# Optimization experiments

Measured on AMD Instinct MI355X. Metric: run time of the kernel, lower is better.

## Reference

```python
import jax, jax.numpy as jnp
import numpy as np

N = 100000
E = 1600000
F_IN = 64
F_OUT = 64
K = 3


def setup_inputs() -> dict:
    key = jax.random.key(0)
    k1, k2, k3, k4, k5 = jax.random.split(key, 5)
    x = jax.random.normal(k1, (N, F_IN), dtype=jnp.float32)
    rows = jnp.sort(jax.random.randint(k2, (E,), 0, N, dtype=jnp.int32))
    cols = jax.random.randint(k3, (E,), 0, N, dtype=jnp.int32)
    vals = jax.random.uniform(k4, (E,), dtype=jnp.float32)
    # xavier-uniform-ish weights
    limit = float(np.sqrt(6.0 / (F_IN + F_OUT)))
    weight = jax.random.uniform(k5, (K, F_IN, F_OUT), dtype=jnp.float32,
                                minval=-limit, maxval=limit)
    bias = jnp.zeros((F_OUT,), dtype=jnp.float32)
    return {"x": x, "rows": rows, "cols": cols, "vals": vals,
            "weight": weight, "bias": bias}


def _spmm(vals, rows, cols, h):
    # adj @ h with adj in COO form: out[i] = sum_{e: rows[e]==i} vals[e] * h[cols[e]]
    return jax.ops.segment_sum(vals[:, None] * h[cols], rows, num_segments=N)


def reference(x, rows, cols, vals, weight, bias):
    Tx_0 = x                              # T_0(L) x = x
    Tx_1 = _spmm(vals, rows, cols, x)     # T_1(L) x = L x
    out = Tx_0 @ weight[0] + Tx_1 @ weight[1]
    for k in range(2, K):                 # Chebyshev recurrence (K is small/static)
        Tx_2 = 2.0 * _spmm(vals, rows, cols, Tx_1) - Tx_0
        out = out + Tx_2 @ weight[k]
        Tx_0, Tx_1 = Tx_1, Tx_2
    return out + bias
```

## Files before the change

kernel.cpp:

```cpp
#include <hip/hip_runtime.h>

constexpr int NN = 100000;
constexpr int NE = 1600000;
constexpr int F  = 64;

typedef short bf16x8 __attribute__((ext_vector_type(8)));
typedef float f32x4  __attribute__((ext_vector_type(4)));

__device__ __forceinline__ float bf_lo(unsigned u) { return __uint_as_float(u << 16); }
__device__ __forceinline__ float bf_hi(unsigned u) { return __uint_as_float(u & 0xFFFF0000u); }
__device__ __forceinline__ unsigned pack_bf16(float a, float b) {
    unsigned ua = __float_as_uint(a);
    unsigned ub = __float_as_uint(b);
    ua = (ua + 0x7FFFu + ((ua >> 16) & 1u)) >> 16;
    ub = (ub + 0x7FFFu + ((ub >> 16) & 1u)) & 0xFFFF0000u;
    return ua | ub;
}

__global__ __launch_bounds__(256)
void build_row_ptr_k(const int* __restrict__ rows, int* __restrict__ row_ptr) {
    int r = blockIdx.x * 256 + threadIdx.x;
    if (r > NN) return;
    int lo = 0, hi = NE;
    while (lo < hi) {
        int mid = (lo + hi) >> 1;
        if (rows[mid] < r) lo = mid + 1; else hi = mid;
    }
    row_ptr[r] = lo;
}

__global__ __launch_bounds__(256)
void cvt_x_k(const float* __restrict__ x, ushort* __restrict__ xb) {
    int tid = blockIdx.x * 256 + threadIdx.x;
    if (tid >= NN * F / 8) return;
    const float4* p = (const float4*)x + (size_t)tid * 2;
    float4 a = p[0], b = p[1];
    uint4 o = make_uint4(pack_bf16(a.x, a.y), pack_bf16(a.z, a.w),
                         pack_bf16(b.x, b.y), pack_bf16(b.z, b.w));
    ((uint4*)xb)[tid] = o;
}

__global__ __launch_bounds__(256)
void cvt_w_k(const float* __restrict__ w, ushort* __restrict__ wt) {
    int tid = blockIdx.x * 256 + threadIdx.x;
    if (tid >= 192 * 64) return;
    int k = tid >> 6, n = tid & 63;
    unsigned u = __float_as_uint(w[tid]);
    u = (u + 0x7FFFu + ((u >> 16) & 1u)) >> 16;
    wt[n * 192 + k] = (ushort)u;
}

template<bool SECOND>
__global__ __launch_bounds__(256)
void spmm_k(const int* __restrict__ row_ptr, const int* __restrict__ cols,
            const float* __restrict__ vals, const ushort* __restrict__ src,
            const ushort* __restrict__ x0, ushort* __restrict__ dst) {
    const int lane = threadIdx.x & 63;
    const int i = blockIdx.x * 4 + (threadIdx.x >> 6);
    if (i >= NN) return;
    const int e0 = row_ptr[i];
    const int e1 = row_ptr[i + 1];
    const int fgrp = lane & 7;
    const int egrp = lane >> 3;
    float acc[8] = {};
    for (int base = e0; base < e1; base += 64) {
        const int n = min(64, e1 - base);
        int c = 0; float v = 0.f;
        if (lane < n) {
            c = cols[base + lane];
            v = vals[base + lane];
        }
        const int steps = (n + 7) >> 3;
        #pragma unroll 4
        for (int s = 0; s < steps; ++s) {
            int   cj = __shfl(c, s * 8 + egrp);
            float vj = __shfl(v, s * 8 + egrp);
            uint4 raw = *(const uint4*)(src + (size_t)cj * F + fgrp * 8);
            acc[0] += vj * bf_lo(raw.x); acc[1] += vj * bf_hi(raw.x);
            acc[2] += vj * bf_lo(raw.y); acc[3] += vj * bf_hi(raw.y);
            acc[4] += vj * bf_lo(raw.z); acc[5] += vj * bf_hi(raw.z);
            acc[6] += vj * bf_lo(raw.w); acc[7] += vj * bf_hi(raw.w);
        }
    }
    #pragma unroll
    for (int m = 8; m < 64; m <<= 1)
        #pragma unroll
        for (int t = 0; t < 8; ++t)
            acc[t] += __shfl_xor(acc[t], m);
    if (egrp == 0) {
        float r[8];
        if (SECOND) {
            uint4 xr = *(const uint4*)(x0 + (size_t)i * F + fgrp * 8);
            r[0] = 2.f * acc[0] - bf_lo(xr.x); r[1] = 2.f * acc[1] - bf_hi(xr.x);
            r[2] = 2.f * acc[2] - bf_lo(xr.y); r[3] = 2.f * acc[3] - bf_hi(xr.y);
            r[4] = 2.f * acc[4] - bf_lo(xr.z); r[5] = 2.f * acc[5] - bf_hi(xr.z);
            r[6] = 2.f * acc[6] - bf_lo(xr.w); r[7] = 2.f * acc[7] - bf_hi(xr.w);
        } else {
            #pragma unroll
            for (int t = 0; t < 8; ++t) r[t] = acc[t];
        }
        uint4 o = make_uint4(pack_bf16(r[0], r[1]), pack_bf16(r[2], r[3]),
                             pack_bf16(r[4], r[5]), pack_bf16(r[6], r[7]));
        *(uint4*)(dst + (size_t)i * F + fgrp * 8) = o;
    }
}

__global__ __launch_bounds__(256)
void dense_k(const ushort* __restrict__ xb, const ushort* __restrict__ t1,
             const ushort* __restrict__ t2, const ushort* __restrict__ wt,
             const float* __restrict__ bias, float* __restrict__ out) {
    const int tid  = threadIdx.x;
    const int lane = tid & 63;
    const int wv   = tid >> 6;
    const int row0 = blockIdx.x * 64 + wv * 16;
    const int m    = lane & 15;
    const int quad = lane >> 4;
    int arow = row0 + m;
    if (arow >= NN) arow = NN - 1;

    f32x4 acc[4] = {};
    #pragma unroll
    for (int kb = 0; kb < 6; ++kb) {
        const int kbase = kb * 32;
        const ushort* seg = (kb < 2) ? xb : (kb < 4) ? t1 : t2;
        const int off = (kbase & 63) + quad * 8;
        bf16x8 a = *(const bf16x8*)(seg + (size_t)arow * F + off);
        #pragma unroll
        for (int t = 0; t < 4; ++t) {
            const int n = t * 16 + m;
            bf16x8 b = *(const bf16x8*)(wt + (size_t)n * 192 + kbase + quad * 8);
            acc[t] = __builtin_amdgcn_mfma_f32_16x16x32_bf16(a, b, acc[t], 0, 0, 0);
        }
    }
    #pragma unroll
    for (int t = 0; t < 4; ++t) {
        const int col = t * 16 + m;
        const float bv = bias[col];
        #pragma unroll
        for (int r = 0; r < 4; ++r) {
            const int grow = row0 + quad * 4 + r;
            if (grow < NN) out[(size_t)grow * F + col] = acc[t][r] + bv;
        }
    }
}

extern "C" void kernel_launch(void* const* d_in, const int* in_sizes, int n_in,
                              void* d_out, int out_size, void* d_ws, size_t ws_size,
                              hipStream_t stream) {
    const float* x    = (const float*)d_in[0];
    const int*   rows = (const int*)  d_in[1];
    const int*   cols = (const int*)  d_in[2];
    const float* vals = (const float*)d_in[3];
    const float* w    = (const float*)d_in[4];
    const float* bias = (const float*)d_in[5];
    float* out = (float*)d_out;

    char* ws = (char*)d_ws;
    int* row_ptr = (int*)ws;
    size_t off = (((size_t)(NN + 1) * sizeof(int)) + 255) & ~(size_t)255;
    ushort* xb  = (ushort*)(ws + off);
    ushort* t1b = xb  + (size_t)NN * F;
    ushort* t2b = t1b + (size_t)NN * F;
    ushort* wt  = t2b + (size_t)NN * F;

    build_row_ptr_k<<<(NN + 1 + 255) / 256, 256, 0, stream>>>(rows, row_ptr);
    cvt_x_k<<<(NN * F / 8 + 255) / 256, 256, 0, stream>>>(x, xb);
    cvt_w_k<<<(192 * 64 + 255) / 256, 256, 0, stream>>>(w, wt);
    spmm_k<false><<<NN / 4, 256, 0, stream>>>(row_ptr, cols, vals, xb,  nullptr, t1b);
    spmm_k<true ><<<NN / 4, 256, 0, stream>>>(row_ptr, cols, vals, t1b, xb,      t2b);
    dense_k<<<(NN + 63) / 64, 256, 0, stream>>>(xb, t1b, t2b, wt, bias, out);
}
```

Baseline: 213.6 us.

## Fuse prep kernels, map eight rows per wave in SpMM, stage dense output via LDS

Merges the x conversion, row_ptr construction and weight transpose into one prep kernel, and builds row_ptr by scanning edges for row boundaries instead of one binary search per row. SpMM now gives each 8-lane group its own row and loops to the wave's maximum degree with masked edges. This removes the cross-lane reduction and raises parallelism for the average degree of 16, at the cost of load imbalance between rows of different degree. The dense kernel stages results through shared memory so each output row is written as contiguous float4 stores.

```diff
diff --git a/kernel.cpp b/kernel.cpp
--- a/kernel.cpp
+++ b/kernel.cpp
@@ -17,37 +17,36 @@
     return ua | ub;
 }
 
-__global__ __launch_bounds__(256)
-void build_row_ptr_k(const int* __restrict__ rows, int* __restrict__ row_ptr) {
-    int r = blockIdx.x * 256 + threadIdx.x;
-    if (r > NN) return;
-    int lo = 0, hi = NE;
-    while (lo < hi) {
-        int mid = (lo + hi) >> 1;
-        if (rows[mid] < r) lo = mid + 1; else hi = mid;
-    }
-    row_ptr[r] = lo;
-}
+constexpr int B_CVT = NN * F / 8 / 256;
+constexpr int B_RP  = NE / 256;
+constexpr int B_W   = 192 * 64 / 256;
 
 __global__ __launch_bounds__(256)
-void cvt_x_k(const float* __restrict__ x, ushort* __restrict__ xb) {
-    int tid = blockIdx.x * 256 + threadIdx.x;
-    if (tid >= NN * F / 8) return;
-    const float4* p = (const float4*)x + (size_t)tid * 2;
-    float4 a = p[0], b = p[1];
-    uint4 o = make_uint4(pack_bf16(a.x, a.y), pack_bf16(a.z, a.w),
-                         pack_bf16(b.x, b.y), pack_bf16(b.z, b.w));
-    ((uint4*)xb)[tid] = o;
-}
-
-__global__ __launch_bounds__(256)
-void cvt_w_k(const float* __restrict__ w, ushort* __restrict__ wt) {
-    int tid = blockIdx.x * 256 + threadIdx.x;
-    if (tid >= 192 * 64) return;
-    int k = tid >> 6, n = tid & 63;
-    unsigned u = __float_as_uint(w[tid]);
-    u = (u + 0x7FFFu + ((u >> 16) & 1u)) >> 16;
-    wt[n * 192 + k] = (ushort)u;
+void prep_k(const float* __restrict__ x, ushort* __restrict__ xb,
+            const int* __restrict__ rows, int* __restrict__ row_ptr,
+            const float* __restrict__ w, ushort* __restrict__ wt) {
+    const int b = blockIdx.x;
+    if (b < B_CVT) {
+        int tid = b * 256 + threadIdx.x;
+        const float4* p = (const float4*)x + (size_t)tid * 2;
+        float4 a = p[0], c = p[1];
+        uint4 o = make_uint4(pack_bf16(a.x, a.y), pack_bf16(a.z, a.w),
+                             pack_bf16(c.x, c.y), pack_bf16(c.z, c.w));
+        ((uint4*)xb)[tid] = o;
+    } else if (b < B_CVT + B_RP) {
+        int e = (b - B_CVT) * 256 + threadIdx.x;
+        int r1 = rows[e];
+        int r2 = (e == NE - 1) ? NN : rows[e + 1];
+        for (int r = r1 + 1; r <= r2; ++r) row_ptr[r] = e + 1;
+        if (e == 0)
+            for (int r = 0; r <= r1; ++r) row_ptr[r] = 0;
+    } else {
+        int tid = (b - B_CVT - B_RP) * 256 + threadIdx.x;
+        int k = tid >> 6, n = tid & 63;
+        unsigned u = __float_as_uint(w[tid]);
+        u = (u + 0x7FFFu + ((u >> 16) & 1u)) >> 16;
+        wt[n * 192 + k] = (ushort)u;
+    }
 }
 
 template<bool SECOND>
@@ -56,59 +55,54 @@
             const float* __restrict__ vals, const ushort* __restrict__ src,
             const ushort* __restrict__ x0, ushort* __restrict__ dst) {
     const int lane = threadIdx.x & 63;
-    const int i = blockIdx.x * 4 + (threadIdx.x >> 6);
-    if (i >= NN) return;
-    const int e0 = row_ptr[i];
-    const int e1 = row_ptr[i + 1];
     const int fgrp = lane & 7;
-    const int egrp = lane >> 3;
+    const int g    = lane >> 3;
+    const int r    = (blockIdx.x * 4 + (threadIdx.x >> 6)) * 8 + g;
+    const int e0 = row_ptr[r];
+    const int e1 = row_ptr[r + 1];
+    const int deg = e1 - e0;
+    int maxdeg = deg;
+    maxdeg = max(maxdeg, __shfl_xor(maxdeg, 8));
+    maxdeg = max(maxdeg, __shfl_xor(maxdeg, 16));
+    maxdeg = max(maxdeg, __shfl_xor(maxdeg, 32));
+
     float acc[8] = {};
-    for (int base = e0; base < e1; base += 64) {
-        const int n = min(64, e1 - base);
-        int c = 0; float v = 0.f;
-        if (lane < n) {
-            c = cols[base + lane];
-            v = vals[base + lane];
-        }
-        const int steps = (n + 7) >> 3;
-        #pragma unroll 4
-        for (int s = 0; s < steps; ++s) {
-            int   cj = __shfl(c, s * 8 + egrp);
-            float vj = __shfl(v, s * 8 + egrp);
-            uint4 raw = *(const uint4*)(src + (size_t)cj * F + fgrp * 8);
-            acc[0] += vj * bf_lo(raw.x); acc[1] += vj * bf_hi(raw.x);
-            acc[2] += vj * bf_lo(raw.y); acc[3] += vj * bf_hi(raw.y);
-            acc[4] += vj * bf_lo(raw.z); acc[5] += vj * bf_hi(raw.z);
-            acc[6] += vj * bf_lo(raw.w); acc[7] += vj * bf_hi(raw.w);
-        }
+    #pragma unroll 2
+    for (int s = 0; s < maxdeg; ++s) {
+        const bool act = s < deg;
+        int ec = act ? (e0 + s) : (e1 - 1);
+        ec = ec < 0 ? 0 : ec;
+        const int   cj = cols[ec];
+        const float vv = vals[ec];
+        const float vj = act ? vv : 0.f;
+        uint4 raw = *(const uint4*)(src + (size_t)cj * F + fgrp * 8);
+        acc[0] += vj * bf_lo(raw.x); acc[1] += vj * bf_hi(raw.x);
+        acc[2] += vj * bf_lo(raw.y); acc[3] += vj * bf_hi(raw.y);
+        acc[4] += vj * bf_lo(raw.z); acc[5] += vj * bf_hi(raw.z);
+        acc[6] += vj * bf_lo(raw.w); acc[7] += vj * bf_hi(raw.w);
     }
-    #pragma unroll
-    for (int m = 8; m < 64; m <<= 1)
+
+    float o[8];
+    if (SECOND) {
+        uint4 xr = *(const uint4*)(x0 + (size_t)r * F + fgrp * 8);
+        o[0] = 2.f * acc[0] - bf_lo(xr.x); o[1] = 2.f * acc[1] - bf_hi(xr.x);
+        o[2] = 2.f * acc[2] - bf_lo(xr.y); o[3] = 2.f * acc[3] - bf_hi(xr.y);
+        o[4] = 2.f * acc[4] - bf_lo(xr.z); o[5] = 2.f * acc[5] - bf_hi(xr.z);
+        o[6] = 2.f * acc[6] - bf_lo(xr.w); o[7] = 2.f * acc[7] - bf_hi(xr.w);
+    } else {
         #pragma unroll
-        for (int t = 0; t < 8; ++t)
-            acc[t] += __shfl_xor(acc[t], m);
-    if (egrp == 0) {
-        float r[8];
-        if (SECOND) {
-            uint4 xr = *(const uint4*)(x0 + (size_t)i * F + fgrp * 8);
-            r[0] = 2.f * acc[0] - bf_lo(xr.x); r[1] = 2.f * acc[1] - bf_hi(xr.x);
-            r[2] = 2.f * acc[2] - bf_lo(xr.y); r[3] = 2.f * acc[3] - bf_hi(xr.y);
-            r[4] = 2.f * acc[4] - bf_lo(xr.z); r[5] = 2.f * acc[5] - bf_hi(xr.z);
-            r[6] = 2.f * acc[6] - bf_lo(xr.w); r[7] = 2.f * acc[7] - bf_hi(xr.w);
-        } else {
-            #pragma unroll
-            for (int t = 0; t < 8; ++t) r[t] = acc[t];
-        }
-        uint4 o = make_uint4(pack_bf16(r[0], r[1]), pack_bf16(r[2], r[3]),
-                             pack_bf16(r[4], r[5]), pack_bf16(r[6], r[7]));
-        *(uint4*)(dst + (size_t)i * F + fgrp * 8) = o;
+        for (int t = 0; t < 8; ++t) o[t] = acc[t];
     }
+    uint4 ov = make_uint4(pack_bf16(o[0], o[1]), pack_bf16(o[2], o[3]),
+                          pack_bf16(o[4], o[5]), pack_bf16(o[6], o[7]));
+    *(uint4*)(dst + (size_t)r * F + fgrp * 8) = ov;
 }
 
 __global__ __launch_bounds__(256)
 void dense_k(const ushort* __restrict__ xb, const ushort* __restrict__ t1,
              const ushort* __restrict__ t2, const ushort* __restrict__ wt,
              const float* __restrict__ bias, float* __restrict__ out) {
+    __shared__ float lds[4][16 * 68];
     const int tid  = threadIdx.x;
     const int lane = tid & 63;
     const int wv   = tid >> 6;
@@ -132,15 +126,24 @@
             acc[t] = __builtin_amdgcn_mfma_f32_16x16x32_bf16(a, b, acc[t], 0, 0, 0);
         }
     }
+
+    float* sl = lds[wv];
     #pragma unroll
     for (int t = 0; t < 4; ++t) {
-        const int col = t * 16 + m;
-        const float bv = bias[col];
+        const float bv = bias[t * 16 + m];
         #pragma unroll
-        for (int r = 0; r < 4; ++r) {
-            const int grow = row0 + quad * 4 + r;
-            if (grow < NN) out[(size_t)grow * F + col] = acc[t][r] + bv;
-        }
+        for (int rr = 0; rr < 4; ++rr)
+            sl[(quad * 4 + rr) * 68 + t * 16 + m] = acc[t][rr] + bv;
+    }
+    __syncthreads();
+    const int m4 = (lane & 15) * 4;
+    #pragma unroll
+    for (int p = 0; p < 4; ++p) {
+        const int rl = p * 4 + (lane >> 4);
+        const int grow = row0 + rl;
+        f32x4 v = *(const f32x4*)(sl + rl * 68 + m4);
+        if (grow < NN)
+            *(f32x4*)(out + (size_t)grow * F + m4) = v;
     }
 }
 
@@ -163,10 +166,8 @@
     ushort* t2b = t1b + (size_t)NN * F;
     ushort* wt  = t2b + (size_t)NN * F;
 
-    build_row_ptr_k<<<(NN + 1 + 255) / 256, 256, 0, stream>>>(rows, row_ptr);
-    cvt_x_k<<<(NN * F / 8 + 255) / 256, 256, 0, stream>>>(x, xb);
-    cvt_w_k<<<(192 * 64 + 255) / 256, 256, 0, stream>>>(w, wt);
-    spmm_k<false><<<NN / 4, 256, 0, stream>>>(row_ptr, cols, vals, xb,  nullptr, t1b);
-    spmm_k<true ><<<NN / 4, 256, 0, stream>>>(row_ptr, cols, vals, t1b, xb,      t2b);
+    prep_k<<<B_CVT + B_RP + B_W, 256, 0, stream>>>(x, xb, rows, row_ptr, w, wt);
+    spmm_k<false><<<NN / 32, 256, 0, stream>>>(row_ptr, cols, vals, xb,  nullptr, t1b);
+    spmm_k<true ><<<NN / 32, 256, 0, stream>>>(row_ptr, cols, vals, t1b, xb,      t2b);
     dense_k<<<(NN + 63) / 64, 256, 0, stream>>>(xb, t1b, t2b, wt, bias, out);
 }
```

Result: faster. 186.1 us (-12.9%).
